# Kernel tuning notes

Measured on AMD Instinct MI355X. Metric: run time of the kernel, lower is better.

## Reference

```python
import jax, jax.numpy as jnp
import numpy as np

N_NODES = 100000
N_EDGES = 1600000
N_GRAPHS = 2000
F_IN = 16
HEADS = 8
C = 16            # per-head out channels (hidden_dim)
HC = HEADS * C    # 128
N_CLASSES = 2
NEG_SLOPE = 0.2   # PyG GATConv default leaky_relu slope


def setup_inputs() -> dict:
    key = jax.random.key(0)
    ks = jax.random.split(key, 12)
    x = jax.random.normal(ks[0], (N_NODES, F_IN), dtype=jnp.float32)
    edge_index = jax.random.randint(ks[1], (2, N_EDGES), 0, N_NODES, dtype=jnp.int32)
    batch = jnp.sort(jax.random.randint(ks[2], (N_NODES,), 0, N_GRAPHS, dtype=jnp.int32))
    s1 = 1.0 / np.sqrt(F_IN)
    s2 = 1.0 / np.sqrt(HC)
    return {
        "x": x,
        "edge_index": edge_index,
        "batch": batch,
        "W1": jax.random.normal(ks[3], (F_IN, HC), dtype=jnp.float32) * s1,
        "a1_src": jax.random.normal(ks[4], (HEADS, C), dtype=jnp.float32) * s2,
        "a1_dst": jax.random.normal(ks[5], (HEADS, C), dtype=jnp.float32) * s2,
        "b1": jnp.zeros((HC,), dtype=jnp.float32),
        "W2": jax.random.normal(ks[6], (HC, HC), dtype=jnp.float32) * s2,
        "a2_src": jax.random.normal(ks[7], (HEADS, C), dtype=jnp.float32) * s2,
        "a2_dst": jax.random.normal(ks[8], (HEADS, C), dtype=jnp.float32) * s2,
        "b2": jnp.zeros((HC,), dtype=jnp.float32),
        "lin_W": jax.random.normal(ks[9], (HC, N_CLASSES), dtype=jnp.float32) * s2,
        "lin_b": jnp.zeros((N_CLASSES,), dtype=jnp.float32),
    }


def gat_layer(h_in, src, dst, W, a_src, a_dst, b, num_nodes):
    # h: [N, H, C] per-head transformed features
    h = (h_in @ W).reshape(num_nodes, HEADS, C)
    # per-node attention half-logits: [N, H]
    logit_src = jnp.einsum('nhc,hc->nh', h, a_src)
    logit_dst = jnp.einsum('nhc,hc->nh', h, a_dst)
    # per-edge logits [E, H]
    e = jax.nn.leaky_relu(logit_src[src] + logit_dst[dst], NEG_SLOPE)
    # segment softmax over incoming edges of each destination node
    m = jax.ops.segment_max(e, dst, num_segments=num_nodes)
    m = jnp.where(jnp.isfinite(m), m, 0.0)
    ex = jnp.exp(e - m[dst])
    denom = jax.ops.segment_sum(ex, dst, num_segments=num_nodes)
    alpha = ex / jnp.maximum(denom[dst], 1e-16)
    # weighted scatter-add aggregation: [N, H, C]
    out = jax.ops.segment_sum(alpha[:, :, None] * h[src], dst, num_segments=num_nodes)
    return out.reshape(num_nodes, HC) + b


def reference(x, edge_index, batch, W1, a1_src, a1_dst, b1, W2, a2_src, a2_dst, b2, lin_W, lin_b):
    n = x.shape[0]
    # PyG GATConv adds self-loops by default
    loops = jnp.arange(n, dtype=edge_index.dtype)
    src = jnp.concatenate([edge_index[0], loops])
    dst = jnp.concatenate([edge_index[1], loops])
    h = jax.nn.relu(gat_layer(x, src, dst, W1, a1_src, a1_dst, b1, n))
    h = jax.nn.relu(gat_layer(h, src, dst, W2, a2_src, a2_dst, b2, n))
    # global mean pool per graph
    sums = jax.ops.segment_sum(h, batch, num_segments=N_GRAPHS)
    counts = jax.ops.segment_sum(jnp.ones((n, 1), h.dtype), batch, num_segments=N_GRAPHS)
    pooled = sums / jnp.maximum(counts, 1.0)
    logits = pooled @ lin_W + lin_b
    return jax.nn.softmax(logits, axis=1)
```

## Files before the change

### kernel.cpp

```cpp
#include <hip/hip_runtime.h>
#include <math.h>

#define N_NODES 100000
#define N_EDGESI 1600000
#define E_TOTAL (N_EDGESI + N_NODES)
#define N_GRAPHS 2000
#define F_IN 16
#define HEADS 8
#define CPH 16
#define HC 128
#define NEG 0.2f

#define BSHIFT 9
#define BNODES (1<<BSHIFT)
#define NBUK ((N_NODES + BNODES - 1)/BNODES)
#define BCAP 12288
#define BIN_EPT 16
#define BIN_TPB 256
#define BIN_EPB (BIN_EPT*BIN_TPB)
#define NBIN_BLK ((E_TOTAL + BIN_EPB - 1)/BIN_EPB)

#define GOFF_BLK ((N_NODES+255)/256)
#define WCONV_BLK ((HC*HC)/256)

typedef __bf16 bf16x8 __attribute__((ext_vector_type(8)));
typedef float  f32x4  __attribute__((ext_vector_type(4)));

__device__ __forceinline__ float leaky(float x){ return fmaxf(x, NEG*x); }
__device__ __forceinline__ float bf2f(unsigned short u){ return __uint_as_float(((unsigned)u)<<16); }
__device__ __forceinline__ unsigned short f2bf(float f){
  unsigned u = __float_as_uint(f);
  unsigned r = (u + 0x7fffu + ((u>>16)&1u)) >> 16;
  return (unsigned short)r;
}
__device__ __forceinline__ float blo(unsigned u){ return __uint_as_float(u<<16); }
__device__ __forceinline__ float bhi(unsigned u){ return __uint_as_float(u & 0xffff0000u); }

__global__ void k_pre(const int* __restrict__ ei, int* __restrict__ gpos, unsigned* __restrict__ gbin,
                      const int* __restrict__ batch, int* __restrict__ goff,
                      const float* __restrict__ W, unsigned short* __restrict__ Wt){
  int blk = blockIdx.x;
  if (blk < NBIN_BLK){
    __shared__ int cnt[NBUK];
    __shared__ int lofs[NBUK];
    __shared__ int bbase[NBUK];
    __shared__ int ws[4];
    __shared__ unsigned sorted[BIN_EPB];
    __shared__ unsigned short sbkt[BIN_EPB];
    int t = threadIdx.x;
    for (int i = t; i < NBUK; i += BIN_TPB) cnt[i] = 0;
    __syncthreads();
    int base = blk*BIN_EPB;
    unsigned entry[BIN_EPT]; int ebkt[BIN_EPT]; int erank[BIN_EPT];
    #pragma unroll
    for (int i = 0; i < BIN_EPT; ++i){
      int e = base + i*BIN_TPB + t;
      if (e < E_TOTAL){
        unsigned s, d;
        if (e < N_EDGESI){ s = (unsigned)ei[e]; d = (unsigned)ei[N_EDGESI + e]; }
        else { s = d = (unsigned)(e - N_EDGESI); }
        int b = (int)(d >> BSHIFT);
        erank[i] = atomicAdd(&cnt[b], 1);
        ebkt[i] = b;
        entry[i] = ((d & (BNODES-1u)) << 17) | s;
      } else ebkt[i] = -1;
    }
    __syncthreads();
    {
      int lane = t & 63, wv = t >> 6;
      int v = (t < NBUK) ? cnt[t] : 0;
      int sc = v;
      #pragma unroll
      for (int o = 1; o < 64; o <<= 1){ int u = __shfl_up(sc, o, 64); if (lane >= o) sc += u; }
      if (lane == 63) ws[wv] = sc;
      __syncthreads();
      if (wv == 0 && lane < 4){
        int w2 = ws[lane];
        #pragma unroll
        for (int o = 1; o < 4; o <<= 1){ int u = __shfl_up(w2, o, 64); if (lane >= o) w2 += u; }
        ws[lane] = w2;
      }
      __syncthreads();
      if (t < NBUK){
        lofs[t] = (wv ? ws[wv-1] : 0) + sc - v;
        bbase[t] = v ? atomicAdd(&gpos[t], v) : 0;
      }
    }
    __syncthreads();
    #pragma unroll
    for (int i = 0; i < BIN_EPT; ++i){
      if (ebkt[i] >= 0){
        int p = lofs[ebkt[i]] + erank[i];
        sorted[p] = entry[i];
        sbkt[p] = (unsigned short)ebkt[i];
      }
    }
    __syncthreads();
    int nval = E_TOTAL - base; if (nval > BIN_EPB) nval = BIN_EPB;
    for (int i = t; i < nval; i += BIN_TPB){
      int b = sbkt[i];
      gbin[(size_t)b*BCAP + bbase[b] + (i - lofs[b])] = sorted[i];
    }
  } else if (blk < NBIN_BLK + GOFF_BLK){
    int n = (blk - NBIN_BLK)*256 + threadIdx.x;
    if (n >= N_NODES) return;
    int b = batch[n];
    if (n == 0){ for (int g = 0; g <= b; ++g) goff[g] = 0; }
    int b1 = (n+1 < N_NODES) ? batch[n+1] : N_GRAPHS;
    for (int g = b+1; g <= b1; ++g) goff[g] = n+1;
  } else {
    int i = (blk - NBIN_BLK - GOFF_BLK)*256 + threadIdx.x;
    if (i >= HC*HC) return;
    int c = i >> 7, k = i & 127;
    Wt[i] = f2bf(W[k*HC + c]);
  }
}

__global__ __launch_bounds__(512) void k_csr(
                      const int* __restrict__ gpos, const unsigned* __restrict__ gbin,
                      int* __restrict__ off, int* __restrict__ csrc){
  __shared__ int lcnt[BNODES];
  __shared__ int wsum[8];
  __shared__ int gp[NBUK];
  __shared__ int sbase;
  int b = blockIdx.x, t = threadIdx.x;
  for (int i = t; i < NBUK; i += 512) gp[i] = gpos[i];
  lcnt[t] = 0;
  __syncthreads();
  if (t == 0){ int s = 0; for (int j = 0; j < b; ++j) s += gp[j]; sbase = s; }
  int nb = gp[b];
  const unsigned* bb = gbin + (size_t)b*BCAP;
  __syncthreads();
  int base = sbase;
  for (int i = t; i < nb; i += 512) atomicAdd(&lcnt[bb[i] >> 17], 1);
  __syncthreads();
  int lane = t & 63, wv = t >> 6;
  int v = lcnt[t];
  int sc = v;
  #pragma unroll
  for (int o = 1; o < 64; o <<= 1){ int u = __shfl_up(sc, o, 64); if (lane >= o) sc += u; }
  if (lane == 63) wsum[wv] = sc;
  __syncthreads();
  if (wv == 0 && lane < 8){
    int w2 = wsum[lane];
    #pragma unroll
    for (int o = 1; o < 8; o <<= 1){ int u = __shfl_up(w2, o, 64); if (lane >= o) w2 += u; }
    wsum[lane] = w2;
  }
  __syncthreads();
  int excl = (wv ? wsum[wv-1] : 0) + sc - v;
  int d = (b << BSHIFT) + t;
  if (d < N_NODES) off[d] = base + excl;
  if (b == NBUK-1 && t == 0) off[N_NODES] = E_TOTAL;
  __syncthreads();
  lcnt[t] = base + excl;
  __syncthreads();
  for (int i = t; i < nb; i += 512){
    unsigned en = bb[i];
    int p = atomicAdd(&lcnt[en >> 17], 1);
    csrc[p] = (int)(en & 0x1ffffu);
  }
}

__global__ __launch_bounds__(256) void k_gemm1(
                        const float* __restrict__ x, const float* __restrict__ W,
                        const float* __restrict__ asrc, const float* __restrict__ adst,
                        unsigned short* __restrict__ hb,
                        float* __restrict__ ls, float* __restrict__ ld){
  int i = blockIdx.x*256 + threadIdx.x;
  if (i >= N_NODES*64) return;
  int n = i >> 6, cp = i & 63;
  const float4* xr4 = (const float4*)(x + n*F_IN);
  float4 x0 = xr4[0], x1 = xr4[1], x2 = xr4[2], x3 = xr4[3];
  float xr[16] = { x0.x,x0.y,x0.z,x0.w, x1.x,x1.y,x1.z,x1.w,
                   x2.x,x2.y,x2.z,x2.w, x3.x,x3.y,x3.z,x3.w };
  const float2* W2v = (const float2*)W;
  float a0 = 0.f, a1 = 0.f;
  #pragma unroll
  for (int k = 0; k < F_IN; ++k){
    float2 wv2 = W2v[k*64 + cp];
    a0 += xr[k]*wv2.x; a1 += xr[k]*wv2.y;
  }
  ushort2 o; o.x = f2bf(a0); o.y = f2bf(a1);
  ((ushort2*)hb)[i] = o;
  int h = cp >> 3;
  int cih = 2*(cp & 7);
  float2 asv = *(const float2*)(asrc + h*CPH + cih);
  float2 adv = *(const float2*)(adst + h*CPH + cih);
  float ps = a0*asv.x + a1*asv.y;
  float pd = a0*adv.x + a1*adv.y;
  #pragma unroll
  for (int o2 = 1; o2 < 8; o2 <<= 1){ ps += __shfl_xor(ps, o2, 64); pd += __shfl_xor(pd, o2, 64); }
  if ((cp & 7) == 0){
    ls[n*8 + h] = ps;
    ld[n*8 + h] = pd;
  }
}

__global__ __launch_bounds__(256) void k_gemm2_mfma(
                             const unsigned short* __restrict__ hin,
                             const unsigned short* __restrict__ w2t,
                             const float* __restrict__ asrc, const float* __restrict__ adst,
                             unsigned short* __restrict__ hb,
                             float* __restrict__ ls, float* __restrict__ ld){
  __shared__ unsigned short hls[64][132];
  int t = threadIdx.x, lane = t & 63, wv = t >> 6;
  int n0 = blockIdx.x*64 + wv*16;
  int rowl = lane & 15, kgrp = lane >> 4;
  int row = n0 + rowl;
  int rowc = (row < N_NODES) ? row : (N_NODES-1);
  bf16x8 a[4];
  #pragma unroll
  for (int ks = 0; ks < 4; ++ks)
    a[ks] = *(const bf16x8*)(hin + (size_t)rowc*HC + ks*32 + kgrp*8);
  #pragma unroll
  for (int ct = 0; ct < 8; ++ct){
    f32x4 acc = {0.f, 0.f, 0.f, 0.f};
    int col = ct*16 + rowl;
    #pragma unroll
    for (int ks = 0; ks < 4; ++ks){
      bf16x8 b = *(const bf16x8*)(w2t + (size_t)col*HC + ks*32 + kgrp*8);
      acc = __builtin_amdgcn_mfma_f32_16x16x32_bf16(a[ks], b, acc, 0, 0, 0);
    }
    #pragma unroll
    for (int r = 0; r < 4; ++r){
      int lrow = wv*16 + kgrp*4 + r;
      int ro = n0 + kgrp*4 + r;
      unsigned short hv = f2bf(acc[r]);
      hls[lrow][col] = hv;
      if (ro < N_NODES) hb[(size_t)ro*HC + col] = hv;
    }
  }
  __syncthreads();
  #pragma unroll
  for (int pp = 0; pp < 2; ++pp){
    int p = t + pp*256;
    int lrow = p >> 3, h = p & 7;
    int gn = blockIdx.x*64 + lrow;
    if (gn < N_NODES){
      const unsigned short* rp = &hls[lrow][h*16];
      uint2 A = *(const uint2*)rp;
      uint2 B = *(const uint2*)(rp+4);
      uint2 C = *(const uint2*)(rp+8);
      uint2 D = *(const uint2*)(rp+12);
      float c[16] = { blo(A.x), bhi(A.x), blo(A.y), bhi(A.y),
                      blo(B.x), bhi(B.x), blo(B.y), bhi(B.y),
                      blo(C.x), bhi(C.x), blo(C.y), bhi(C.y),
                      blo(D.x), bhi(D.x), blo(D.y), bhi(D.y) };
      const float* as = asrc + h*CPH;
      const float* ad = adst + h*CPH;
      float s0 = 0.f, s1 = 0.f;
      #pragma unroll
      for (int q = 0; q < 16; ++q){ s0 += c[q]*as[q]; s1 += c[q]*ad[q]; }
      ls[gn*8 + h] = s0;
      ld[gn*8 + h] = s1;
    }
  }
}

__global__ void k_agg(const int* __restrict__ off, const int* __restrict__ csrc,
                      const unsigned short* __restrict__ hb, const float* __restrict__ ls,
                      const float* __restrict__ ld, const float* __restrict__ bias,
                      unsigned short* __restrict__ outb){
  int wid = threadIdx.x >> 6, lane = threadIdx.x & 63;
  int n = blockIdx.x*4 + wid;
  if (n >= N_NODES) return;
  int rs = __builtin_amdgcn_readfirstlane(off[n]);
  int re = __builtin_amdgcn_readfirstlane(off[n+1]);
  int q = lane >> 4;
  int l = lane & 15;
  int h = l >> 1;
  float ldh = ld[n*8 + h];
  const uint4* hb4 = (const uint4*)hb;
  float ac0=0.f, ac1=0.f, ac2=0.f, ac3=0.f, ac4=0.f, ac5=0.f, ac6=0.f, ac7=0.f, dsum=0.f;
  #define AGG_BODY(J) { \
    int s = __shfl(sv, (J), 64); \
    float g = ls[s*8 + h]; \
    float ex = __expf(leaky(g + ldh)); \
    uint4 v = hb4[(size_t)s*16 + l]; \
    ac0 += ex*blo(v.x); ac1 += ex*bhi(v.x); \
    ac2 += ex*blo(v.y); ac3 += ex*bhi(v.y); \
    ac4 += ex*blo(v.z); ac5 += ex*bhi(v.z); \
    ac6 += ex*blo(v.w); ac7 += ex*bhi(v.w); \
    dsum += ex; }
  int nb = re - rs;
  for (int cb = 0; cb < nb; cb += 64){
    int cnt = nb - cb; if (cnt > 64) cnt = 64;
    int sv = csrc[rs + cb + (lane < cnt ? lane : 0)];
    int jj = 0;
    for (; jj + 16 <= cnt; jj += 16){
      AGG_BODY(jj+q) AGG_BODY(jj+q+4) AGG_BODY(jj+q+8) AGG_BODY(jj+q+12)
    }
    for (int j = jj + q; j < cnt; j += 4) AGG_BODY(j)
  }
  #undef AGG_BODY
  ac0 += __shfl_xor(ac0,16,64); ac0 += __shfl_xor(ac0,32,64);
  ac1 += __shfl_xor(ac1,16,64); ac1 += __shfl_xor(ac1,32,64);
  ac2 += __shfl_xor(ac2,16,64); ac2 += __shfl_xor(ac2,32,64);
  ac3 += __shfl_xor(ac3,16,64); ac3 += __shfl_xor(ac3,32,64);
  ac4 += __shfl_xor(ac4,16,64); ac4 += __shfl_xor(ac4,32,64);
  ac5 += __shfl_xor(ac5,16,64); ac5 += __shfl_xor(ac5,32,64);
  ac6 += __shfl_xor(ac6,16,64); ac6 += __shfl_xor(ac6,32,64);
  ac7 += __shfl_xor(ac7,16,64); ac7 += __shfl_xor(ac7,32,64);
  dsum += __shfl_xor(dsum,16,64); dsum += __shfl_xor(dsum,32,64);
  if (q == 0){
    float inv = 1.f/fmaxf(dsum, 1e-16f);
    float4 b0 = ((const float4*)bias)[l*2];
    float4 b1 = ((const float4*)bias)[l*2+1];
    uint4 o;
    o.x = (unsigned)f2bf(fmaxf(ac0*inv + b0.x, 0.f)) | ((unsigned)f2bf(fmaxf(ac1*inv + b0.y, 0.f)) << 16);
    o.y = (unsigned)f2bf(fmaxf(ac2*inv + b0.z, 0.f)) | ((unsigned)f2bf(fmaxf(ac3*inv + b0.w, 0.f)) << 16);
    o.z = (unsigned)f2bf(fmaxf(ac4*inv + b1.x, 0.f)) | ((unsigned)f2bf(fmaxf(ac5*inv + b1.y, 0.f)) << 16);
    o.w = (unsigned)f2bf(fmaxf(ac6*inv + b1.z, 0.f)) | ((unsigned)f2bf(fmaxf(ac7*inv + b1.w, 0.f)) << 16);
    ((uint4*)outb)[(size_t)n*16 + l] = o;
  }
}

__global__ void k_poolcls(const unsigned short* __restrict__ h, const int* __restrict__ goff,
                          const float* __restrict__ lw, const float* __restrict__ lb,
                          float* __restrict__ out){
  __shared__ float sh[4][HC];
  int g = blockIdx.x;
  int t = threadIdx.x, lane = t & 63, wv = t >> 6;
  int s = goff[g], epos = goff[g+1];
  float a0 = 0.f, a1 = 0.f;
  const ushort2* h2 = (const ushort2*)h;
  for (int n = s + wv; n < epos; n += 4){
    ushort2 v = h2[(size_t)n*64 + lane];
    a0 += bf2f(v.x); a1 += bf2f(v.y);
  }
  sh[wv][lane*2] = a0; sh[wv][lane*2+1] = a1;
  __syncthreads();
  if (wv == 0){
    int c0 = lane*2;
    float p0 = sh[0][c0] + sh[1][c0] + sh[2][c0] + sh[3][c0];
    float p1 = sh[0][c0+1] + sh[1][c0+1] + sh[2][c0+1] + sh[3][c0+1];
    int cntg = epos - s;
    float invc = 1.f/fmaxf((float)cntg, 1.f);
    float v0 = p0*invc, v1 = p1*invc;
    float l0 = v0*lw[c0*2+0] + v1*lw[(c0+1)*2+0];
    float l1 = v0*lw[c0*2+1] + v1*lw[(c0+1)*2+1];
    #pragma unroll
    for (int o = 32; o >= 1; o >>= 1){ l0 += __shfl_xor(l0,o,64); l1 += __shfl_xor(l1,o,64); }
    if (lane == 0){
      l0 += lb[0]; l1 += lb[1];
      float m = fmaxf(l0,l1);
      float e0 = __expf(l0-m), e1 = __expf(l1-m);
      float si = e0 + e1;
      out[g*2]   = e0/si;
      out[g*2+1] = e1/si;
    }
  }
}

extern "C" void kernel_launch(void* const* d_in, const int* in_sizes, int n_in,
                              void* d_out, int out_size, void* d_ws, size_t ws_size,
                              hipStream_t stream){
  const float* x   = (const float*)d_in[0];
  const int*   ei  = (const int*)d_in[1];
  const int*   bat = (const int*)d_in[2];
  const float* W1  = (const float*)d_in[3];
  const float* a1s = (const float*)d_in[4];
  const float* a1d = (const float*)d_in[5];
  const float* b1  = (const float*)d_in[6];
  const float* W2  = (const float*)d_in[7];
  const float* a2s = (const float*)d_in[8];
  const float* a2d = (const float*)d_in[9];
  const float* b2  = (const float*)d_in[10];
  const float* lw  = (const float*)d_in[11];
  const float* lb  = (const float*)d_in[12];
  float* out = (float*)d_out;

  char* w = (char*)d_ws;
  auto alloc = [&](size_t bytes)->void*{ void* p = (void*)w; w += (bytes + 511) & ~size_t(511); return p; };
  int* off    = (int*)alloc((size_t)(N_NODES+1)*4);
  int* csrc   = (int*)alloc((size_t)E_TOTAL*4);
  int* goff   = (int*)alloc((size_t)(N_GRAPHS+1)*4);
  int* gpos   = (int*)alloc((size_t)NBUK*4);
  unsigned* gbin = (unsigned*)alloc((size_t)NBUK*BCAP*4);
  unsigned short* w2t  = (unsigned short*)alloc((size_t)HC*HC*2);
  unsigned short* hbf  = (unsigned short*)alloc((size_t)N_NODES*HC*2);
  unsigned short* hbf2 = (unsigned short*)alloc((size_t)N_NODES*HC*2);
  float* lsb  = (float*)alloc((size_t)N_NODES*HEADS*4);
  float* ldb  = (float*)alloc((size_t)N_NODES*HEADS*4);

  hipMemsetAsync(gpos, 0, (size_t)NBUK*4, stream);

  k_pre  <<<NBIN_BLK + GOFF_BLK + WCONV_BLK,BIN_TPB,0,stream>>>(ei, gpos, gbin, bat, goff, W2, w2t);
  k_gemm1<<<(N_NODES*64)/256,256,0,stream>>>(x, W1, a1s, a1d, hbf, lsb, ldb);
  k_csr  <<<NBUK,512,0,stream>>>(gpos, gbin, off, csrc);

  k_agg  <<<(N_NODES+3)/4,256,0,stream>>>(off, csrc, hbf, lsb, ldb, b1, hbf2);
  k_gemm2_mfma<<<(N_NODES+63)/64,256,0,stream>>>(hbf2, w2t, a2s, a2d, hbf, lsb, ldb);
  k_agg  <<<(N_NODES+3)/4,256,0,stream>>>(off, csrc, hbf, lsb, ldb, b2, hbf2);

  k_poolcls<<<N_GRAPHS,256,0,stream>>>(hbf2, goff, lw, lb, out);
}
```

Measured before the change: 313.2 us.

## Run layer-1 projection on MFMA via bf16 padded x and templated GEMM

Replaces the scalar fp32 first-layer GEMM kernel with the MFMA GEMM kernel, now templated on K-steps, fed by bf16 copies of x (zero-padded from 16 to 32 features) and a transposed, padded bf16 W1 built inside the preprocessing kernel. It also halves the edges handled per thread in the binning blocks, which doubles the number of binning blocks. The MFMA path replaces many scalar FMAs, but it adds a conversion pass that writes a padded x buffer and rounds x to bf16, which costs some precision.

```diff
diff --git a/kernel.cpp b/kernel.cpp
--- a/kernel.cpp
+++ b/kernel.cpp
@@ -15,13 +15,15 @@
 #define BNODES (1<<BSHIFT)
 #define NBUK ((N_NODES + BNODES - 1)/BNODES)
 #define BCAP 12288
-#define BIN_EPT 16
+#define BIN_EPT 8
 #define BIN_TPB 256
 #define BIN_EPB (BIN_EPT*BIN_TPB)
 #define NBIN_BLK ((E_TOTAL + BIN_EPB - 1)/BIN_EPB)
 
 #define GOFF_BLK ((N_NODES+255)/256)
 #define WCONV_BLK ((HC*HC)/256)
+#define XCONV_BLK ((N_NODES*4 + 255)/256)
+#define W1CONV_BLK ((HC*32)/256)
 
 typedef __bf16 bf16x8 __attribute__((ext_vector_type(8)));
 typedef float  f32x4  __attribute__((ext_vector_type(4)));
@@ -38,7 +40,9 @@
 
 __global__ void k_pre(const int* __restrict__ ei, int* __restrict__ gpos, unsigned* __restrict__ gbin,
                       const int* __restrict__ batch, int* __restrict__ goff,
-                      const float* __restrict__ W, unsigned short* __restrict__ Wt){
+                      const float* __restrict__ W2, unsigned short* __restrict__ w2t,
+                      const float* __restrict__ x, unsigned short* __restrict__ xbf,
+                      const float* __restrict__ W1, unsigned short* __restrict__ w1t){
   int blk = blockIdx.x;
   if (blk < NBIN_BLK){
     __shared__ int cnt[NBUK];
@@ -75,10 +79,10 @@
       if (lane == 63) ws[wv] = sc;
       __syncthreads();
       if (wv == 0 && lane < 4){
-        int w2 = ws[lane];
+        int w2v = ws[lane];
         #pragma unroll
-        for (int o = 1; o < 4; o <<= 1){ int u = __shfl_up(w2, o, 64); if (lane >= o) w2 += u; }
-        ws[lane] = w2;
+        for (int o = 1; o < 4; o <<= 1){ int u = __shfl_up(w2v, o, 64); if (lane >= o) w2v += u; }
+        ws[lane] = w2v;
       }
       __syncthreads();
       if (t < NBUK){
@@ -108,11 +112,25 @@
     if (n == 0){ for (int g = 0; g <= b; ++g) goff[g] = 0; }
     int b1 = (n+1 < N_NODES) ? batch[n+1] : N_GRAPHS;
     for (int g = b+1; g <= b1; ++g) goff[g] = n+1;
-  } else {
+  } else if (blk < NBIN_BLK + GOFF_BLK + WCONV_BLK){
     int i = (blk - NBIN_BLK - GOFF_BLK)*256 + threadIdx.x;
     if (i >= HC*HC) return;
     int c = i >> 7, k = i & 127;
-    Wt[i] = f2bf(W[k*HC + c]);
+    w2t[i] = f2bf(W2[k*HC + c]);
+  } else if (blk < NBIN_BLK + GOFF_BLK + WCONV_BLK + XCONV_BLK){
+    int p = (blk - NBIN_BLK - GOFF_BLK - WCONV_BLK)*256 + threadIdx.x;
+    if (p >= N_NODES*4) return;
+    int n = p >> 2, q = p & 3;
+    float4 xv = ((const float4*)(x + n*F_IN))[q];
+    ushort4 o; o.x = f2bf(xv.x); o.y = f2bf(xv.y); o.z = f2bf(xv.z); o.w = f2bf(xv.w);
+    ((ushort4*)(xbf + (size_t)n*32))[q] = o;
+    ushort4 z; z.x = 0; z.y = 0; z.z = 0; z.w = 0;
+    ((ushort4*)(xbf + (size_t)n*32 + 16))[q] = z;
+  } else {
+    int i = (blk - NBIN_BLK - GOFF_BLK - WCONV_BLK - XCONV_BLK)*256 + threadIdx.x;
+    if (i >= HC*32) return;
+    int c = i >> 5, k = i & 31;
+    w1t[i] = (k < F_IN) ? f2bf(W1[k*HC + c]) : (unsigned short)0;
   }
 }
 
@@ -162,64 +180,31 @@
   }
 }
 
-__global__ __launch_bounds__(256) void k_gemm1(
-                        const float* __restrict__ x, const float* __restrict__ W,
-                        const float* __restrict__ asrc, const float* __restrict__ adst,
-                        unsigned short* __restrict__ hb,
-                        float* __restrict__ ls, float* __restrict__ ld){
-  int i = blockIdx.x*256 + threadIdx.x;
-  if (i >= N_NODES*64) return;
-  int n = i >> 6, cp = i & 63;
-  const float4* xr4 = (const float4*)(x + n*F_IN);
-  float4 x0 = xr4[0], x1 = xr4[1], x2 = xr4[2], x3 = xr4[3];
-  float xr[16] = { x0.x,x0.y,x0.z,x0.w, x1.x,x1.y,x1.z,x1.w,
-                   x2.x,x2.y,x2.z,x2.w, x3.x,x3.y,x3.z,x3.w };
-  const float2* W2v = (const float2*)W;
-  float a0 = 0.f, a1 = 0.f;
-  #pragma unroll
-  for (int k = 0; k < F_IN; ++k){
-    float2 wv2 = W2v[k*64 + cp];
-    a0 += xr[k]*wv2.x; a1 += xr[k]*wv2.y;
-  }
-  ushort2 o; o.x = f2bf(a0); o.y = f2bf(a1);
-  ((ushort2*)hb)[i] = o;
-  int h = cp >> 3;
-  int cih = 2*(cp & 7);
-  float2 asv = *(const float2*)(asrc + h*CPH + cih);
-  float2 adv = *(const float2*)(adst + h*CPH + cih);
-  float ps = a0*asv.x + a1*asv.y;
-  float pd = a0*adv.x + a1*adv.y;
-  #pragma unroll
-  for (int o2 = 1; o2 < 8; o2 <<= 1){ ps += __shfl_xor(ps, o2, 64); pd += __shfl_xor(pd, o2, 64); }
-  if ((cp & 7) == 0){
-    ls[n*8 + h] = ps;
-    ld[n*8 + h] = pd;
-  }
-}
-
-__global__ __launch_bounds__(256) void k_gemm2_mfma(
+template<int KS>
+__global__ __launch_bounds__(256) void k_gemm_mfma(
                              const unsigned short* __restrict__ hin,
-                             const unsigned short* __restrict__ w2t,
+                             const unsigned short* __restrict__ wt,
                              const float* __restrict__ asrc, const float* __restrict__ adst,
                              unsigned short* __restrict__ hb,
                              float* __restrict__ ls, float* __restrict__ ld){
   __shared__ unsigned short hls[64][132];
+  const int KST = KS*32;
   int t = threadIdx.x, lane = t & 63, wv = t >> 6;
   int n0 = blockIdx.x*64 + wv*16;
   int rowl = lane & 15, kgrp = lane >> 4;
   int row = n0 + rowl;
   int rowc = (row < N_NODES) ? row : (N_NODES-1);
-  bf16x8 a[4];
+  bf16x8 a[KS];
   #pragma unroll
-  for (int ks = 0; ks < 4; ++ks)
-    a[ks] = *(const bf16x8*)(hin + (size_t)rowc*HC + ks*32 + kgrp*8);
+  for (int ks = 0; ks < KS; ++ks)
+    a[ks] = *(const bf16x8*)(hin + (size_t)rowc*KST + ks*32 + kgrp*8);
   #pragma unroll
   for (int ct = 0; ct < 8; ++ct){
     f32x4 acc = {0.f, 0.f, 0.f, 0.f};
     int col = ct*16 + rowl;
     #pragma unroll
-    for (int ks = 0; ks < 4; ++ks){
-      bf16x8 b = *(const bf16x8*)(w2t + (size_t)col*HC + ks*32 + kgrp*8);
+    for (int ks = 0; ks < KS; ++ks){
+      bf16x8 b = *(const bf16x8*)(wt + (size_t)col*KST + ks*32 + kgrp*8);
       acc = __builtin_amdgcn_mfma_f32_16x16x32_bf16(a[ks], b, acc, 0, 0, 0);
     }
     #pragma unroll
@@ -379,6 +364,8 @@
   int* gpos   = (int*)alloc((size_t)NBUK*4);
   unsigned* gbin = (unsigned*)alloc((size_t)NBUK*BCAP*4);
   unsigned short* w2t  = (unsigned short*)alloc((size_t)HC*HC*2);
+  unsigned short* w1t  = (unsigned short*)alloc((size_t)HC*32*2);
+  unsigned short* xbf  = (unsigned short*)alloc((size_t)N_NODES*32*2);
   unsigned short* hbf  = (unsigned short*)alloc((size_t)N_NODES*HC*2);
   unsigned short* hbf2 = (unsigned short*)alloc((size_t)N_NODES*HC*2);
   float* lsb  = (float*)alloc((size_t)N_NODES*HEADS*4);
@@ -386,12 +373,13 @@
 
   hipMemsetAsync(gpos, 0, (size_t)NBUK*4, stream);
 
-  k_pre  <<<NBIN_BLK + GOFF_BLK + WCONV_BLK,BIN_TPB,0,stream>>>(ei, gpos, gbin, bat, goff, W2, w2t);
-  k_gemm1<<<(N_NODES*64)/256,256,0,stream>>>(x, W1, a1s, a1d, hbf, lsb, ldb);
+  k_pre  <<<NBIN_BLK + GOFF_BLK + WCONV_BLK + XCONV_BLK + W1CONV_BLK,BIN_TPB,0,stream>>>(
+           ei, gpos, gbin, bat, goff, W2, w2t, x, xbf, W1, w1t);
+  k_gemm_mfma<1><<<(N_NODES+63)/64,256,0,stream>>>(xbf, w1t, a1s, a1d, hbf, lsb, ldb);
   k_csr  <<<NBUK,512,0,stream>>>(gpos, gbin, off, csrc);
 
   k_agg  <<<(N_NODES+3)/4,256,0,stream>>>(off, csrc, hbf, lsb, ldb, b1, hbf2);
-  k_gemm2_mfma<<<(N_NODES+63)/64,256,0,stream>>>(hbf2, w2t, a2s, a2d, hbf, lsb, ldb);
+  k_gemm_mfma<4><<<(N_NODES+63)/64,256,0,stream>>>(hbf2, w2t, a2s, a2d, hbf, lsb, ldb);
   k_agg  <<<(N_NODES+3)/4,256,0,stream>>>(off, csrc, hbf, lsb, ldb, b2, hbf2);
 
   k_poolcls<<<N_GRAPHS,256,0,stream>>>(hbf2, goff, lw, lb, out);
```

Result: faster. 270.1 us (-13.8%).
